# Performance work log

Measured on AMD Instinct MI355X. Metric: run time of the kernel, lower is better.

Reference implementation:

```python
import jax, jax.numpy as jnp
import numpy as np

S = 3136        # tokens (56x56 patch grid, single image segment -> full attention)
H = 16          # num_heads
D = 80          # head_dim (= head_dim_ori = PADDING_HEAD_DIM)
HID = H * D     # 1280
SCALE = 1.0 / float(np.sqrt(D))  # qkScale = 1/sqrt(head_dim_ori)


def _rope_tables(s, d, base=10000.0):
    # rotate_half style: cos/sin of shape [s, d], duplicated over the two halves
    half = d // 2
    inv_freq = 1.0 / (base ** (np.arange(0, half, dtype=np.float32) / half))
    freqs = np.outer(np.arange(s, dtype=np.float32), inv_freq)  # [s, d/2]
    emb = np.concatenate([freqs, freqs], axis=-1)               # [s, d]
    return jnp.asarray(np.cos(emb)), jnp.asarray(np.sin(emb))


def setup_inputs() -> dict:
    key = jax.random.key(0)
    ks = jax.random.split(key, 6)
    cos, sin = _rope_tables(S, D)
    return {
        "hidden_states": jax.random.normal(ks[0], (S, HID), jnp.float32),
        "x_norm": jax.random.normal(ks[1], (S, HID), jnp.float32),
        "qkv_w": jax.random.normal(ks[2], (3 * HID, HID), jnp.float32) * 0.02,
        "qkv_b": jax.random.normal(ks[3], (3 * HID,), jnp.float32) * 0.02,
        "proj_w": jax.random.normal(ks[4], (HID, HID), jnp.float32) * 0.02,
        "proj_b": jax.random.normal(ks[5], (HID,), jnp.float32) * 0.02,
        "cos": cos,
        "sin": sin,
    }


def _rotate_half(x):
    x1, x2 = jnp.split(x, 2, axis=-1)
    return jnp.concatenate([-x2, x1], axis=-1)


def reference(hidden_states, x_norm, qkv_w, qkv_b, proj_w, proj_b, cos, sin):
    # fused QKV linear (transposeB=True) + split into q,k,v along last dim
    qkv = x_norm @ qkv_w.T + qkv_b                      # [S, 3*HID]
    q, k, v = jnp.split(qkv, 3, axis=-1)                # each [S, HID]
    q = q.reshape(S, H, D)
    k = k.reshape(S, H, D)
    v = v.reshape(S, H, D)
    # inline RoPE on q and k (rotate_half over full head_dim)
    c = cos[:, None, :]; s = sin[:, None, :]           # [S,1,D]
    q = q * c + _rotate_half(q) * s
    k = k * c + _rotate_half(k) * s
    # full self-attention (PA_ENCODER, single segment = seq_len S)
    scores = jnp.einsum('shd,thd->hst', q, k) * SCALE   # [H,S,S]
    probs = jax.nn.softmax(scores, axis=-1)
    attn = jnp.einsum('hst,thd->shd', probs, v)         # [S,H,D]
    attn = attn.reshape(S, HID)
    # output projection + residual add
    out = attn @ proj_w.T + proj_b
    return hidden_states + out
```

## Files before the change

### kernel.cpp

```cpp
#include <hip/hip_runtime.h>
#include <hip/hip_bf16.h>

#define S_   3136
#define H_   16
#define D_   80
#define DP_  96
#define HID_ 1280

typedef short  bf16x8 __attribute__((ext_vector_type(8)));
typedef short  bf16x4 __attribute__((ext_vector_type(4)));
typedef float  f32x4  __attribute__((ext_vector_type(4)));

__device__ __forceinline__ float b2f(unsigned short u) {
    union { unsigned int i; float f; } c;
    c.i = ((unsigned int)u) << 16;
    return c.f;
}
__device__ __forceinline__ unsigned short f2b(float f) {
    union { unsigned int i; float f; } c;
    c.f = f;
    unsigned int x = c.i;
    unsigned int lsb = (x >> 16) & 1u;
    x += 0x7fffu + lsb;
    return (unsigned short)(x >> 16);
}
__device__ __forceinline__ unsigned int cvt_pk_bf16(float lo, float hi) {
    unsigned int r;
    asm("v_cvt_pk_bf16_f32 %0, %1, %2" : "=v"(r) : "v"(lo), "v"(hi));
    return r;
}

typedef const void __attribute__((address_space(1))) GAS;
typedef void __attribute__((address_space(3))) LAS;
__device__ __forceinline__ void gl16(const void* g, void* l) {
    __builtin_amdgcn_global_load_lds((GAS*)g, (LAS*)l, 16, 0, 0);
}

#define N4_X 1003520
#define N4_Q 1228800
#define N4_P 409600

__global__ __launch_bounds__(256)
void cast3_kernel(const float* __restrict__ x0, unsigned short* __restrict__ y0,
                  const float* __restrict__ x1, unsigned short* __restrict__ y1,
                  const float* __restrict__ x2, unsigned short* __restrict__ y2)
{
    int i = blockIdx.x * 256 + threadIdx.x;
    const float* src; unsigned short* dst;
    if (i < N4_X)               { src = x0; dst = y0; }
    else if (i < N4_X + N4_Q)   { src = x1; dst = y1; i -= N4_X; }
    else if (i < N4_X + N4_Q + N4_P) { src = x2; dst = y2; i -= N4_X + N4_Q; }
    else return;
    float4 v = ((const float4*)src)[i];
    ushort4 o;
    o.x = f2b(v.x); o.y = f2b(v.y); o.z = f2b(v.z); o.w = f2b(v.w);
    ((ushort4*)dst)[i] = o;
}

#define ASTR 40

__global__ __launch_bounds__(256)
void qkv_mfma_kernel(const unsigned short* __restrict__ Ab,
                     const unsigned short* __restrict__ Wb,
                     const float* __restrict__ bias,
                     unsigned short* __restrict__ qo, unsigned short* __restrict__ ko,
                     unsigned short* __restrict__ vtb)
{
    __shared__ __align__(16) short As[2][128][ASTR];
    __shared__ __align__(16) short Bs[2][128][ASTR];
    int m0 = blockIdx.x * 128;
    int n0 = blockIdx.y * 128;
    int t = threadIdx.x;
    int wave = t >> 6, lane = t & 63, lq = lane & 15, quad = lane >> 4;
    int wr = wave >> 1, wc = wave & 1;

    int r0  = t >> 2;
    int r1  = r0 + 64;
    int kc0 = (t & 3) << 3;
    const unsigned short* pa0 = Ab + (size_t)min(m0 + r0, S_ - 1) * HID_ + kc0;
    const unsigned short* pa1 = Ab + (size_t)min(m0 + r1, S_ - 1) * HID_ + kc0;
    const unsigned short* pb0 = Wb + (size_t)(n0 + r0) * HID_ + kc0;
    const unsigned short* pb1 = Wb + (size_t)(n0 + r1) * HID_ + kc0;

    const bf16x8* afp[2][4]; const bf16x8* bfp[2][4];
    #pragma unroll
    for (int s = 0; s < 2; ++s)
        #pragma unroll
        for (int i = 0; i < 4; ++i) {
            afp[s][i] = (const bf16x8*)&As[s][wr * 64 + i * 16 + lq][quad * 8];
            bfp[s][i] = (const bf16x8*)&Bs[s][wc * 64 + i * 16 + lq][quad * 8];
        }

    f32x4 acc[4][4];
    #pragma unroll
    for (int i = 0; i < 4; ++i)
        #pragma unroll
        for (int j = 0; j < 4; ++j) acc[i][j] = (f32x4){0.f, 0.f, 0.f, 0.f};

    bf16x8 va[2][2], vb[2][2];
    #pragma unroll
    for (int s = 0; s < 2; ++s) {
        va[s][0] = *(const bf16x8*)(pa0 + s * 32);
        va[s][1] = *(const bf16x8*)(pa1 + s * 32);
        vb[s][0] = *(const bf16x8*)(pb0 + s * 32);
        vb[s][1] = *(const bf16x8*)(pb1 + s * 32);
    }

    for (int kt = 0; kt < HID_; kt += 64) {
        __syncthreads();
        #pragma unroll
        for (int s = 0; s < 2; ++s) {
            *(bf16x8*)&As[s][r0][kc0] = va[s][0];
            *(bf16x8*)&As[s][r1][kc0] = va[s][1];
            *(bf16x8*)&Bs[s][r0][kc0] = vb[s][0];
            *(bf16x8*)&Bs[s][r1][kc0] = vb[s][1];
        }
        __syncthreads();
        if (kt + 64 < HID_) {
            #pragma unroll
            for (int s = 0; s < 2; ++s) {
                va[s][0] = *(const bf16x8*)(pa0 + kt + 64 + s * 32);
                va[s][1] = *(const bf16x8*)(pa1 + kt + 64 + s * 32);
                vb[s][0] = *(const bf16x8*)(pb0 + kt + 64 + s * 32);
                vb[s][1] = *(const bf16x8*)(pb1 + kt + 64 + s * 32);
            }
        }
        #pragma unroll
        for (int s = 0; s < 2; ++s) {
            bf16x8 af[4], bfr[4];
            #pragma unroll
            for (int i = 0; i < 4; ++i) af[i]  = *afp[s][i];
            #pragma unroll
            for (int j = 0; j < 4; ++j) bfr[j] = *bfp[s][j];
            #pragma unroll
            for (int i = 0; i < 4; ++i)
                #pragma unroll
                for (int j = 0; j < 4; ++j)
                    acc[i][j] = __builtin_amdgcn_mfma_f32_16x16x32_bf16(af[i], bfr[j], acc[i][j], 0, 0, 0);
        }
    }

    #pragma unroll
    for (int i = 0; i < 4; ++i)
        #pragma unroll
        for (int j = 0; j < 4; ++j)
            #pragma unroll
            for (int reg = 0; reg < 4; ++reg) {
                int row = m0 + wr * 64 + i * 16 + quad * 4 + reg;
                if (row >= S_) continue;
                int col = n0 + wc * 64 + j * 16 + lq;
                float val = acc[i][j][reg] + bias[col];
                int which = col / HID_;
                int rem   = col - which * HID_;
                int h     = rem / D_;
                int d     = rem - h * D_;
                if (which == 0)      qo[((size_t)h * S_ + row) * D_ + d] = f2b(val);
                else if (which == 1) ko[((size_t)h * S_ + row) * D_ + d] = f2b(val);
                else                 vtb[((size_t)h * D_ + d) * S_ + row] = f2b(val);
            }
}

__global__ __launch_bounds__(256)
void proj_mfma_kernel(const unsigned short* __restrict__ Ab,
                      const unsigned short* __restrict__ Wb,
                      const float* __restrict__ bias, const float* __restrict__ hidden,
                      float* __restrict__ out)
{
    __shared__ __align__(16) short As[64][ASTR];
    __shared__ __align__(16) short Bs[64][ASTR];
    int m0 = blockIdx.x * 64;
    int n0 = blockIdx.y * 64;
    int t = threadIdx.x;
    int wave = t >> 6, lane = t & 63, lq = lane & 15, quad = lane >> 4;
    int wr = wave >> 1, wc = wave & 1;

    int r  = t >> 2;
    int kc0 = (t & 3) << 3;
    const unsigned short* pa = Ab + (size_t)(m0 + r) * HID_ + kc0;
    const unsigned short* pb = Wb + (size_t)(n0 + r) * HID_ + kc0;
    short* sa = &As[r][kc0];
    short* sb = &Bs[r][kc0];

    const bf16x8* afp[2]; const bf16x8* bfp[2];
    #pragma unroll
    for (int i = 0; i < 2; ++i) {
        afp[i] = (const bf16x8*)&As[wr * 32 + i * 16 + lq][quad * 8];
        bfp[i] = (const bf16x8*)&Bs[wc * 32 + i * 16 + lq][quad * 8];
    }

    f32x4 acc[2][2];
    #pragma unroll
    for (int i = 0; i < 2; ++i)
        #pragma unroll
        for (int j = 0; j < 2; ++j) acc[i][j] = (f32x4){0.f, 0.f, 0.f, 0.f};

    bf16x8 va = *(const bf16x8*)(pa);
    bf16x8 vb = *(const bf16x8*)(pb);

    for (int kt = 0; kt < HID_; kt += 32) {
        __syncthreads();
        *(bf16x8*)sa = va;
        *(bf16x8*)sb = vb;
        __syncthreads();
        if (kt + 32 < HID_) {
            va = *(const bf16x8*)(pa + kt + 32);
            vb = *(const bf16x8*)(pb + kt + 32);
        }
        bf16x8 af[2], bfr[2];
        #pragma unroll
        for (int i = 0; i < 2; ++i) af[i]  = *afp[i];
        #pragma unroll
        for (int j = 0; j < 2; ++j) bfr[j] = *bfp[j];
        #pragma unroll
        for (int i = 0; i < 2; ++i)
            #pragma unroll
            for (int j = 0; j < 2; ++j)
                acc[i][j] = __builtin_amdgcn_mfma_f32_16x16x32_bf16(af[i], bfr[j], acc[i][j], 0, 0, 0);
    }

    #pragma unroll
    for (int i = 0; i < 2; ++i)
        #pragma unroll
        for (int j = 0; j < 2; ++j)
            #pragma unroll
            for (int reg = 0; reg < 4; ++reg) {
                int row = m0 + wr * 32 + i * 16 + quad * 4 + reg;
                int col = n0 + wc * 32 + j * 16 + lq;
                out[(size_t)row * HID_ + col] =
                    acc[i][j][reg] + bias[col] + hidden[(size_t)row * HID_ + col];
            }
}

__global__ void rope_kernel(const unsigned short* __restrict__ q, const unsigned short* __restrict__ k,
                            const float* __restrict__ cost, const float* __restrict__ sint,
                            unsigned short* __restrict__ qb, unsigned short* __restrict__ kb)
{
    const float QSCALE = 0.11180339887498949f * 1.4426950408889634f;
    int idx = blockIdx.x * 256 + threadIdx.x;
    const int total = H_ * S_ * 40;
    if (idx >= total) return;
    int d  = idx % 40;
    int hs = idx / 40;
    int s  = hs % S_;
    size_t base  = (size_t)hs * D_;
    size_t base9 = (size_t)hs * DP_;
    float c1 = cost[s * D_ + d];
    float s1 = sint[s * D_ + d];
    float c2 = cost[s * D_ + d + 40];
    float s2 = sint[s * D_ + d + 40];
    float x1 = b2f(q[base + d]), x2 = b2f(q[base + d + 40]);
    qb[base9 + d]      = f2b((x1 * c1 - x2 * s1) * QSCALE);
    qb[base9 + d + 40] = f2b((x2 * c2 + x1 * s2) * QSCALE);
    x1 = b2f(k[base + d]); x2 = b2f(k[base + d + 40]);
    kb[base9 + d]      = f2b(x1 * c1 - x2 * s1);
    kb[base9 + d + 40] = f2b(x2 * c2 + x1 * s2);
    if (d < 16) {
        qb[base9 + 80 + d] = 0;
        kb[base9 + 80 + d] = 0;
    }
}

#define KBUF_ 16384
#define VBUF_ 10240
#define BUF_  26624

__global__ __launch_bounds__(256, 3)
void attn_kernel(const unsigned short* __restrict__ Qb,
                 const unsigned short* __restrict__ Kb,
                 const unsigned short* __restrict__ Vtb,
                 unsigned short* __restrict__ attnb)
{
    __shared__ __align__(16) unsigned char smem[2 * BUF_];

    int h   = blockIdx.y;
    int qb0 = blockIdx.x * 64;
    int t      = threadIdx.x;
    int wave   = t >> 6;
    int lane   = t & 63;
    int lq     = lane & 15;
    int quad   = lane >> 4;
    int qh     = wave & 1;
    int stripe = wave >> 1;
    int Q0     = qb0 + qh * 32;
    int swz    = (lq & 7) << 4;

    bf16x8 qf[2][3];
    #pragma unroll
    for (int qt = 0; qt < 2; ++qt)
        #pragma unroll
        for (int kc = 0; kc < 3; ++kc)
            qf[qt][kc] = *(const bf16x8*)(Qb + ((size_t)h * S_ + Q0 + qt * 16 + lq) * DP_ + kc * 32 + quad * 8);

    f32x4 O[2][5];
    #pragma unroll
    for (int qt = 0; qt < 2; ++qt)
        #pragma unroll
        for (int dt = 0; dt < 5; ++dt) O[qt][dt] = (f32x4){0.f, 0.f, 0.f, 0.f};
    float l_acc[2] = {0.f, 0.f};

    const unsigned char* kS[4]; int kD[4];
    #pragma unroll
    for (int ii = 0; ii < 4; ++ii) {
        int i  = wave * 4 + ii;
        int rl = i * 4 + (lane >> 4);
        kS[ii] = (const unsigned char*)(Kb + ((size_t)h * S_ + rl) * DP_)
               + (((lane & 15) * 16) ^ ((rl & 7) << 4));
        kD[ii] = i * 1024;
    }
    const unsigned char* vS[3]; int vD[3];
    int nv = (wave < 2) ? 3 : 2;
    #pragma unroll
    for (int jj = 0; jj < 3; ++jj) {
        int j = (jj < 2) ? (wave + jj * 4) : (8 + wave);
        int d = j * 8 + (lane >> 3);
        vS[jj] = (const unsigned char*)(Vtb + (size_t)(h * D_ + d) * S_)
               + (((lane & 7) * 16) ^ ((d & 7) << 4));
        vD[jj] = KBUF_ + j * 1024;
    }

    #define STAGE(bufoff, rr)                                                   \
        do {                                                                    \
            size_t kadv = (size_t)(rr) * (64 * DP_ * 2);                        \
            size_t vadv = (size_t)(rr) * 128;                                   \
            _Pragma("unroll")                                                   \
            for (int ii = 0; ii < 4; ++ii)                                      \
                gl16(kS[ii] + kadv, smem + (bufoff) + kD[ii]);                  \
            _Pragma("unroll")                                                   \
            for (int jj = 0; jj < 3; ++jj)                                      \
                if (jj < nv) gl16(vS[jj] + vadv, smem + (bufoff) + vD[jj]);     \
        } while (0)

    STAGE(0, 0);
    asm volatile("s_waitcnt vmcnt(0)" ::: "memory");
    __syncthreads();

    int cur = 0;
    for (int r = 0; r < 49; ++r) {
        if (r < 48) STAGE(cur ^ BUF_, r + 1);

        const unsigned char* Kbase = smem + cur;
        const unsigned char* Vbase = Kbase + KBUF_;

        f32x4 sc[2][2];
        #pragma unroll
        for (int kt = 0; kt < 2; ++kt) {
            const unsigned char* kbp = Kbase + (stripe * 32 + kt * 16 + lq) * 256;
            bf16x8 kf0 = *(const bf16x8*)(kbp + ((  0 + quad * 16) ^ swz));
            bf16x8 kf1 = *(const bf16x8*)(kbp + (( 64 + quad * 16) ^ swz));
            bf16x8 kf2 = *(const bf16x8*)(kbp + ((128 + quad * 16) ^ swz));
            #pragma unroll
            for (int qt = 0; qt < 2; ++qt) {
                f32x4 a = (f32x4){0.f, 0.f, 0.f, 0.f};
                a = __builtin_amdgcn_mfma_f32_16x16x32_bf16(kf0, qf[qt][0], a, 0, 0, 0);
                a = __builtin_amdgcn_mfma_f32_16x16x32_bf16(kf1, qf[qt][1], a, 0, 0, 0);
                a = __builtin_amdgcn_mfma_f32_16x16x32_bf16(kf2, qf[qt][2], a, 0, 0, 0);
                sc[qt][kt] = a;
            }
        }

        union PaU { bf16x8 v8; unsigned int d[4]; } pa[2];
        #pragma unroll
        for (int qt = 0; qt < 2; ++qt) {
            float e00 = exp2f(sc[qt][0][0]), e01 = exp2f(sc[qt][0][1]);
            float e02 = exp2f(sc[qt][0][2]), e03 = exp2f(sc[qt][0][3]);
            float e10 = exp2f(sc[qt][1][0]), e11 = exp2f(sc[qt][1][1]);
            float e12 = exp2f(sc[qt][1][2]), e13 = exp2f(sc[qt][1][3]);
            l_acc[qt] += ((e00 + e01) + (e02 + e03)) + ((e10 + e11) + (e12 + e13));
            pa[qt].d[0] = cvt_pk_bf16(e00, e01);
            pa[qt].d[1] = cvt_pk_bf16(e02, e03);
            pa[qt].d[2] = cvt_pk_bf16(e10, e11);
            pa[qt].d[3] = cvt_pk_bf16(e12, e13);
        }

        #pragma unroll
        for (int dt = 0; dt < 5; ++dt) {
            const unsigned char* vbp = Vbase + (dt * 16 + lq) * 128;
            union { bf16x8 v8; bf16x4 v4[2]; } vv;
            vv.v4[0] = *(const bf16x4*)(vbp + ((stripe * 64 +      quad * 8) ^ swz));
            vv.v4[1] = *(const bf16x4*)(vbp + ((stripe * 64 + 32 + quad * 8) ^ swz));
            #pragma unroll
            for (int qt = 0; qt < 2; ++qt)
                O[qt][dt] = __builtin_amdgcn_mfma_f32_16x16x32_bf16(pa[qt].v8, vv.v8, O[qt][dt], 0, 0, 0);
        }

        asm volatile("s_waitcnt vmcnt(0)" ::: "memory");
        __syncthreads();
        cur ^= BUF_;
    }
    #undef STAGE

    float lr[2];
    #pragma unroll
    for (int qt = 0; qt < 2; ++qt) {
        float l = l_acc[qt];
        l += __shfl_xor(l, 16);
        l += __shfl_xor(l, 32);
        lr[qt] = l;
    }
    f32x4* Of = (f32x4*)smem;
    float* Lf = (float*)(smem + 20480);
    if (stripe == 1) {
        #pragma unroll
        for (int qt = 0; qt < 2; ++qt) {
            #pragma unroll
            for (int dt = 0; dt < 5; ++dt)
                Of[((qh * 2 + qt) * 5 + dt) * 64 + lane] = O[qt][dt];
            if (lane < 16) Lf[(qh * 2 + qt) * 16 + lane] = lr[qt];
        }
    }
    __syncthreads();
    if (stripe == 0) {
        #pragma unroll
        for (int qt = 0; qt < 2; ++qt) {
            float ltot = lr[qt] + Lf[(qh * 2 + qt) * 16 + lq];
            #pragma unroll
            for (int dt = 0; dt < 5; ++dt)
                O[qt][dt] += Of[((qh * 2 + qt) * 5 + dt) * 64 + lane];
            #pragma unroll
            for (int reg = 0; reg < 4; ++reg) {
                float l = __shfl(ltot, quad * 4 + reg, 16);
                float linv = 1.0f / l;
                int s = Q0 + qt * 16 + quad * 4 + reg;
                unsigned short* orow = attnb + (size_t)s * HID_ + h * D_;
                #pragma unroll
                for (int dt = 0; dt < 5; ++dt)
                    orow[dt * 16 + lq] = f2b(O[qt][dt][reg] * linv);
            }
        }
    }
}

extern "C" void kernel_launch(void* const* d_in, const int* in_sizes, int n_in,
                              void* d_out, int out_size, void* d_ws, size_t ws_size,
                              hipStream_t stream)
{
    const float* hidden = (const float*)d_in[0];
    const float* x_norm = (const float*)d_in[1];
    const float* qkv_w  = (const float*)d_in[2];
    const float* qkv_b  = (const float*)d_in[3];
    const float* proj_w = (const float*)d_in[4];
    const float* proj_b = (const float*)d_in[5];
    const float* cost   = (const float*)d_in[6];
    const float* sint   = (const float*)d_in[7];
    float* out = (float*)d_out;

    unsigned short* w      = (unsigned short*)d_ws;
    unsigned short* qbuf   = w;
    unsigned short* kbuf   = qbuf + 4014080;
    unsigned short* vtb    = kbuf + 4014080;
    unsigned short* kbb    = vtb + 4064256;
    unsigned short* xb     = kbb + 4816896;
    unsigned short* wqkvb  = xb + 4014080;
    unsigned short* wprojb = wqkvb + 4915200;
    unsigned short* qbb    = wqkvb;
    unsigned short* abuf   = qbuf;

    cast3_kernel<<<(N4_X + N4_Q + N4_P + 255) / 256, 256, 0, stream>>>(
        x_norm, xb, qkv_w, wqkvb, proj_w, wprojb);

    qkv_mfma_kernel<<<dim3(25, 30), 256, 0, stream>>>(xb, wqkvb, qkv_b, qbuf, kbuf, vtb);
    rope_kernel<<<(H_ * S_ * 40 + 255) / 256, 256, 0, stream>>>(qbuf, kbuf, cost, sint, qbb, kbb);
    attn_kernel<<<dim3(S_ / 64, H_), 256, 0, stream>>>(qbb, kbb, vtb, abuf);
    proj_mfma_kernel<<<dim3(49, 20), 256, 0, stream>>>(abuf, wprojb, proj_b, hidden, out);
}
```

Before: 315.9 us.

## Load V fragments directly from global into registers, stage only K in LDS

V^T tiles are no longer staged through shared memory. Each lane reads its 5 MFMA V fragments directly from global memory with 8-byte loads at the start of each iteration, and only K stays double-buffered in LDS. The loop is also unrolled by two with fixed buffer offsets, which removes the runtime buffer toggle. This shrinks LDS per block and drops the LDS write/read round trip for V. In exchange it issues many small, poorly coalesced global loads whose latency sits on the critical path before the PV MFMAs.

Result: slower. 510.6 us (+61.6%).

```diff
diff --git a/kernel.cpp b/kernel.cpp
--- a/kernel.cpp
+++ b/kernel.cpp
@@ -261,8 +261,6 @@
 }
 
 #define KBUF_ 16384
-#define VBUF_ 10240
-#define BUF_  26624
 
 __global__ __launch_bounds__(256, 3)
 void attn_kernel(const unsigned short* __restrict__ Qb,
@@ -270,7 +268,7 @@
                  const unsigned short* __restrict__ Vtb,
                  unsigned short* __restrict__ attnb)
 {
-    __shared__ __align__(16) unsigned char smem[2 * BUF_];
+    __shared__ __align__(16) unsigned char smem[2 * KBUF_];
 
     int h   = blockIdx.y;
     int qb0 = blockIdx.x * 64;
@@ -298,96 +296,92 @@
         for (int dt = 0; dt < 5; ++dt) O[qt][dt] = (f32x4){0.f, 0.f, 0.f, 0.f};
     float l_acc[2] = {0.f, 0.f};
 
-    const unsigned char* kS[4]; int kD[4];
+    const unsigned char* kp[4]; int kD[4];
     #pragma unroll
     for (int ii = 0; ii < 4; ++ii) {
         int i  = wave * 4 + ii;
         int rl = i * 4 + (lane >> 4);
-        kS[ii] = (const unsigned char*)(Kb + ((size_t)h * S_ + rl) * DP_)
+        kp[ii] = (const unsigned char*)(Kb + ((size_t)h * S_ + rl) * DP_)
                + (((lane & 15) * 16) ^ ((rl & 7) << 4));
         kD[ii] = i * 1024;
     }
-    const unsigned char* vS[3]; int vD[3];
-    int nv = (wave < 2) ? 3 : 2;
-    #pragma unroll
-    for (int jj = 0; jj < 3; ++jj) {
-        int j = (jj < 2) ? (wave + jj * 4) : (8 + wave);
-        int d = j * 8 + (lane >> 3);
-        vS[jj] = (const unsigned char*)(Vtb + (size_t)(h * D_ + d) * S_)
-               + (((lane & 7) * 16) ^ ((d & 7) << 4));
-        vD[jj] = KBUF_ + j * 1024;
-    }
-
-    #define STAGE(bufoff, rr)                                                   \
-        do {                                                                    \
-            size_t kadv = (size_t)(rr) * (64 * DP_ * 2);                        \
-            size_t vadv = (size_t)(rr) * 128;                                   \
-            _Pragma("unroll")                                                   \
-            for (int ii = 0; ii < 4; ++ii)                                      \
-                gl16(kS[ii] + kadv, smem + (bufoff) + kD[ii]);                  \
-            _Pragma("unroll")                                                   \
-            for (int jj = 0; jj < 3; ++jj)                                      \
-                if (jj < nv) gl16(vS[jj] + vadv, smem + (bufoff) + vD[jj]);     \
-        } while (0)
-
-    STAGE(0, 0);
+
+    const unsigned char* vp[5];
+    {
+        int koff = (stripe * 32 + quad * 4) * 2;
+        #pragma unroll
+        for (int dt = 0; dt < 5; ++dt)
+            vp[dt] = (const unsigned char*)(Vtb + (size_t)(h * D_ + dt * 16 + lq) * S_) + koff;
+    }
+
+    #pragma unroll
+    for (int ii = 0; ii < 4; ++ii)
+        gl16(kp[ii], smem + kD[ii]);
     asm volatile("s_waitcnt vmcnt(0)" ::: "memory");
     __syncthreads();
 
-    int cur = 0;
-    for (int r = 0; r < 49; ++r) {
-        if (r < 48) STAGE(cur ^ BUF_, r + 1);
-
-        const unsigned char* Kbase = smem + cur;
-        const unsigned char* Vbase = Kbase + KBUF_;
-
-        f32x4 sc[2][2];
-        #pragma unroll
-        for (int kt = 0; kt < 2; ++kt) {
-            const unsigned char* kbp = Kbase + (stripe * 32 + kt * 16 + lq) * 256;
-            bf16x8 kf0 = *(const bf16x8*)(kbp + ((  0 + quad * 16) ^ swz));
-            bf16x8 kf1 = *(const bf16x8*)(kbp + (( 64 + quad * 16) ^ swz));
-            bf16x8 kf2 = *(const bf16x8*)(kbp + ((128 + quad * 16) ^ swz));
-            #pragma unroll
-            for (int qt = 0; qt < 2; ++qt) {
-                f32x4 a = (f32x4){0.f, 0.f, 0.f, 0.f};
-                a = __builtin_amdgcn_mfma_f32_16x16x32_bf16(kf0, qf[qt][0], a, 0, 0, 0);
-                a = __builtin_amdgcn_mfma_f32_16x16x32_bf16(kf1, qf[qt][1], a, 0, 0, 0);
-                a = __builtin_amdgcn_mfma_f32_16x16x32_bf16(kf2, qf[qt][2], a, 0, 0, 0);
-                sc[qt][kt] = a;
-            }
-        }
-
-        union PaU { bf16x8 v8; unsigned int d[4]; } pa[2];
-        #pragma unroll
-        for (int qt = 0; qt < 2; ++qt) {
-            float e00 = exp2f(sc[qt][0][0]), e01 = exp2f(sc[qt][0][1]);
-            float e02 = exp2f(sc[qt][0][2]), e03 = exp2f(sc[qt][0][3]);
-            float e10 = exp2f(sc[qt][1][0]), e11 = exp2f(sc[qt][1][1]);
-            float e12 = exp2f(sc[qt][1][2]), e13 = exp2f(sc[qt][1][3]);
-            l_acc[qt] += ((e00 + e01) + (e02 + e03)) + ((e10 + e11) + (e12 + e13));
-            pa[qt].d[0] = cvt_pk_bf16(e00, e01);
-            pa[qt].d[1] = cvt_pk_bf16(e02, e03);
-            pa[qt].d[2] = cvt_pk_bf16(e10, e11);
-            pa[qt].d[3] = cvt_pk_bf16(e12, e13);
-        }
-
-        #pragma unroll
-        for (int dt = 0; dt < 5; ++dt) {
-            const unsigned char* vbp = Vbase + (dt * 16 + lq) * 128;
-            union { bf16x8 v8; bf16x4 v4[2]; } vv;
-            vv.v4[0] = *(const bf16x4*)(vbp + ((stripe * 64 +      quad * 8) ^ swz));
-            vv.v4[1] = *(const bf16x4*)(vbp + ((stripe * 64 + 32 + quad * 8) ^ swz));
-            #pragma unroll
-            for (int qt = 0; qt < 2; ++qt)
-                O[qt][dt] = __builtin_amdgcn_mfma_f32_16x16x32_bf16(pa[qt].v8, vv.v8, O[qt][dt], 0, 0, 0);
-        }
-
-        asm volatile("s_waitcnt vmcnt(0)" ::: "memory");
-        __syncthreads();
-        cur ^= BUF_;
-    }
-    #undef STAGE
+#define BODY(CUROFF, NXTOFF, DO_STAGE)                                          \
+    {                                                                           \
+        union VvU { bf16x8 v8; uint2 u2[2]; } vv[5];                            \
+        _Pragma("unroll")                                                       \
+        for (int dt = 0; dt < 5; ++dt) {                                        \
+            vv[dt].u2[0] = *(const uint2*)(vp[dt]);                             \
+            vv[dt].u2[1] = *(const uint2*)(vp[dt] + 32);                        \
+            vp[dt] += 128;                                                      \
+        }                                                                       \
+        if (DO_STAGE) {                                                         \
+            _Pragma("unroll")                                                   \
+            for (int ii = 0; ii < 4; ++ii) {                                    \
+                kp[ii] += 12288;                                                \
+                gl16(kp[ii], smem + (NXTOFF) + kD[ii]);                         \
+            }                                                                   \
+        }                                                                       \
+        f32x4 sc[2][2];                                                         \
+        _Pragma("unroll")                                                       \
+        for (int kt = 0; kt < 2; ++kt) {                                        \
+            const unsigned char* kbp = smem + (CUROFF)                          \
+                                     + (stripe * 32 + kt * 16 + lq) * 256;      \
+            bf16x8 kf0 = *(const bf16x8*)(kbp + ((  0 + quad * 16) ^ swz));     \
+            bf16x8 kf1 = *(const bf16x8*)(kbp + (( 64 + quad * 16) ^ swz));     \
+            bf16x8 kf2 = *(const bf16x8*)(kbp + ((128 + quad * 16) ^ swz));     \
+            _Pragma("unroll")                                                   \
+            for (int qt = 0; qt < 2; ++qt) {                                    \
+                f32x4 a = (f32x4){0.f, 0.f, 0.f, 0.f};                          \
+                a = __builtin_amdgcn_mfma_f32_16x16x32_bf16(kf0, qf[qt][0], a, 0, 0, 0); \
+                a = __builtin_amdgcn_mfma_f32_16x16x32_bf16(kf1, qf[qt][1], a, 0, 0, 0); \
+                a = __builtin_amdgcn_mfma_f32_16x16x32_bf16(kf2, qf[qt][2], a, 0, 0, 0); \
+                sc[qt][kt] = a;                                                 \
+            }                                                                   \
+        }                                                                       \
+        union PaU { bf16x8 v8; unsigned int d[4]; } pa[2];                      \
+        _Pragma("unroll")                                                       \
+        for (int qt = 0; qt < 2; ++qt) {                                        \
+            float e00 = exp2f(sc[qt][0][0]), e01 = exp2f(sc[qt][0][1]);         \
+            float e02 = exp2f(sc[qt][0][2]), e03 = exp2f(sc[qt][0][3]);         \
+            float e10 = exp2f(sc[qt][1][0]), e11 = exp2f(sc[qt][1][1]);         \
+            float e12 = exp2f(sc[qt][1][2]), e13 = exp2f(sc[qt][1][3]);         \
+            l_acc[qt] += ((e00 + e01) + (e02 + e03)) + ((e10 + e11) + (e12 + e13)); \
+            pa[qt].d[0] = cvt_pk_bf16(e00, e01);                                \
+            pa[qt].d[1] = cvt_pk_bf16(e02, e03);                                \
+            pa[qt].d[2] = cvt_pk_bf16(e10, e11);                                \
+            pa[qt].d[3] = cvt_pk_bf16(e12, e13);                                \
+        }                                                                       \
+        _Pragma("unroll")                                                       \
+        for (int dt = 0; dt < 5; ++dt) {                                        \
+            _Pragma("unroll")                                                   \
+            for (int qt = 0; qt < 2; ++qt)                                      \
+                O[qt][dt] = __builtin_amdgcn_mfma_f32_16x16x32_bf16(pa[qt].v8, vv[dt].v8, O[qt][dt], 0, 0, 0); \
+        }                                                                       \
+        asm volatile("s_waitcnt vmcnt(0)" ::: "memory");                        \
+        __syncthreads();                                                        \
+    }
+
+    for (int rr = 0; rr < 24; ++rr) {
+        BODY(0,     KBUF_, true);
+        BODY(KBUF_, 0,     true);
+    }
+    BODY(0, KBUF_, false);
+#undef BODY
 
     float lr[2];
     #pragma unroll
```
